# Kernel optimization log

Measured on AMD Instinct MI355X. Metric: run time of the kernel, lower is better.

Reference implementation:

```python
import jax, jax.numpy as jnp
import numpy as np

N = 50000
E = 800000
IN_F = 128
OUT_F = 64
HEADS = 4
NEG_SLOPE = 0.2
EPS = 1e-8


def setup_inputs() -> dict:
    key = jax.random.key(0)
    k1, k2, k3, k4, k5 = jax.random.split(key, 5)
    x = jax.random.normal(k1, (N, IN_F), dtype=jnp.float32)
    edge_index = jax.random.randint(k2, (2, E), 0, N, dtype=jnp.int64)
    # xavier-uniform-like scales
    wb = float(np.sqrt(6.0 / (IN_F + OUT_F)))
    ab = float(np.sqrt(6.0 / (OUT_F + 1)))
    W = jax.random.uniform(k3, (HEADS, IN_F, OUT_F), dtype=jnp.float32, minval=-wb, maxval=wb)
    a_src = jax.random.uniform(k4, (HEADS, OUT_F, 1), dtype=jnp.float32, minval=-ab, maxval=ab)
    a_dst = jax.random.uniform(k5, (HEADS, OUT_F, 1), dtype=jnp.float32, minval=-ab, maxval=ab)
    return {"x": x, "edge_index": edge_index, "W": W, "a_src": a_src, "a_dst": a_dst}


def reference(x, edge_index, W, a_src, a_dst):
    n = x.shape[0]
    src, dst = edge_index[0], edge_index[1]
    # per-head projection: (H, N, F)
    Wh = jnp.einsum('ni,hif->hnf', x, W)
    e_src = jnp.einsum('hnf,hf->hn', Wh, a_src[..., 0])
    e_dst = jnp.einsum('hnf,hf->hn', Wh, a_dst[..., 0])
    e = jax.nn.leaky_relu(e_src[:, src] + e_dst[:, dst], NEG_SLOPE)  # (H, E)
    # edge softmax over destination; original initializes e_max to zeros,
    # so effective max is max(segment_max, 0)
    seg_max = jax.vmap(lambda eh: jax.ops.segment_max(eh, dst, num_segments=n))(e)
    e_max = jnp.maximum(seg_max, 0.0)
    exp_e = jnp.exp(e - e_max[:, dst])
    exp_sum = jax.vmap(lambda ee: jax.ops.segment_sum(ee, dst, num_segments=n))(exp_e)
    att = exp_e / (exp_sum[:, dst] + EPS)  # (H, E); dropout omitted (eval)
    # weighted scatter-add aggregation: (H, E, F) messages -> (H, N, F)
    msgs = att[..., None] * Wh[:, src]
    out = jax.vmap(lambda m: jax.ops.segment_sum(m, dst, num_segments=n))(msgs)
    # concat heads: (N, H*F)
    return out.transpose(1, 0, 2).reshape(n, -1)
```

## Files before the change

kernel.cpp:

```cpp
#include <hip/hip_runtime.h>
#include <hip/hip_bf16.h>

#define N_NODES 50000
#define E_EDGES 800000
#define IN_F    128
#define OUT_F   64
#define HEADS   4
#define HF      (HEADS * OUT_F)
#define NEG_SLOPE 0.2f
#define EPS     1e-8f
#define CAP     64
#define NB_INIT ((N_NODES + 255) / 256)

typedef __attribute__((ext_vector_type(8))) short bf16x8;
typedef __attribute__((ext_vector_type(4))) float f32x4;

__device__ __forceinline__ unsigned short f2bf(float f) {
    return __hip_bfloat16_raw(__float2bfloat16(f)).x;
}
__device__ __forceinline__ float bf2f(unsigned short u) {
    return __uint_as_float((unsigned)u << 16);
}

__global__ __launch_bounds__(256) void wcvt_kernel(
    const float* __restrict__ W,
    short* __restrict__ Wtb,
    int* __restrict__ cnt)
{
    const int i = blockIdx.x * 256 + threadIdx.x;
    if (i < N_NODES) cnt[i] = 0;
    if (i < HEADS * IN_F * OUT_F) {
        const int h  = i >> 13;
        const int fl = (i >> 7) & 63;
        const int k  = i & 127;
        Wtb[i] = (short)f2bf(W[h * (IN_F * OUT_F) + k * OUT_F + fl]);
    }
}

__global__ __launch_bounds__(256) void proj_kernel(
    const float* __restrict__ x,
    const short* __restrict__ Wtb,
    const float* __restrict__ a_src,
    const float* __restrict__ a_dst,
    const int* __restrict__ src,
    const int* __restrict__ dst,
    unsigned short* __restrict__ Whb,
    float* __restrict__ esrc,
    float* __restrict__ edst,
    int* __restrict__ cnt,
    int* __restrict__ csr)
{
    __shared__ short xs[16][136];
    __shared__ unsigned short ot[16][256];

    const int tid = threadIdx.x;
    const int n0 = blockIdx.x * 16;

    const int e  = blockIdx.x * 256 + tid;
    const int de = dst[e];
    const int se = src[e];
    const int pos = atomicAdd(&cnt[de], 1);

    {
        const int row = tid >> 4;
        const int kb = (tid & 15) * 8;
        const float* xp = x + (size_t)(n0 + row) * IN_F + kb;
        const float4 x0 = *(const float4*)(xp);
        const float4 x1 = *(const float4*)(xp + 4);
        bf16x8 v;
        v[0] = (short)f2bf(x0.x); v[1] = (short)f2bf(x0.y);
        v[2] = (short)f2bf(x0.z); v[3] = (short)f2bf(x0.w);
        v[4] = (short)f2bf(x1.x); v[5] = (short)f2bf(x1.y);
        v[6] = (short)f2bf(x1.z); v[7] = (short)f2bf(x1.w);
        *(bf16x8*)&xs[row][kb] = v;
    }
    __syncthreads();

    const int h = tid >> 6;
    const int lane = tid & 63;
    const int c = lane & 15;
    const int quad = lane >> 4;

    bf16x8 a[4];
#pragma unroll
    for (int ks = 0; ks < 4; ++ks)
        a[ks] = *(const bf16x8*)&xs[c][ks * 32 + quad * 8];

    f32x4 acc[4];
#pragma unroll
    for (int nt = 0; nt < 4; ++nt) acc[nt] = (f32x4){0.f, 0.f, 0.f, 0.f};

    const short* Wh_head = Wtb + (h << 13);
#pragma unroll
    for (int nt = 0; nt < 4; ++nt) {
        const short* wrow = Wh_head + ((nt * 16 + c) << 7) + (quad << 3);
#pragma unroll
        for (int ks = 0; ks < 4; ++ks) {
            const bf16x8 b = *(const bf16x8*)(wrow + (ks << 5));
            acc[nt] = __builtin_amdgcn_mfma_f32_16x16x32_bf16(a[ks], b, acc[nt], 0, 0, 0);
        }
    }

    float ps[4] = {0.f, 0.f, 0.f, 0.f};
    float pd[4] = {0.f, 0.f, 0.f, 0.f};
#pragma unroll
    for (int nt = 0; nt < 4; ++nt) {
        const float as = a_src[h * OUT_F + nt * 16 + c];
        const float ad = a_dst[h * OUT_F + nt * 16 + c];
#pragma unroll
        for (int r = 0; r < 4; ++r) {
            ps[r] += acc[nt][r] * as;
            pd[r] += acc[nt][r] * ad;
        }
    }
#pragma unroll
    for (int m = 1; m < 16; m <<= 1) {
#pragma unroll
        for (int r = 0; r < 4; ++r) {
            ps[r] += __shfl_xor(ps[r], m);
            pd[r] += __shfl_xor(pd[r], m);
        }
    }
    if (c == 0) {
#pragma unroll
        for (int r = 0; r < 4; ++r) {
            const int n = n0 + quad * 4 + r;
            esrc[n * HEADS + h] = ps[r];
            edst[n * HEADS + h] = pd[r];
        }
    }

#pragma unroll
    for (int nt = 0; nt < 4; ++nt) {
#pragma unroll
        for (int r = 0; r < 4; ++r)
            ot[quad * 4 + r][(nt * 16 + c) * 4 + h] = f2bf(acc[nt][r]);
    }
    __syncthreads();
    {
        const unsigned short* sp = &ot[0][0] + tid * 16;
        unsigned short* gp = Whb + (size_t)n0 * HF + tid * 16;
        *(int4*)(gp)     = *(const int4*)(sp);
        *(int4*)(gp + 8) = *(const int4*)(sp + 8);
    }

    if (pos < CAP) csr[de * CAP + pos] = se;
}

__global__ __launch_bounds__(256) void aggregate_kernel(
    const int* __restrict__ cnt,
    const int* __restrict__ csr,
    const float* __restrict__ esrc,
    const float* __restrict__ edst,
    const unsigned short* __restrict__ Whb,
    float* __restrict__ out)
{
    __shared__ int   sb[4][64];
    __shared__ float pb[4][64][4];

    const int wid = threadIdx.x >> 6;
    const int lane = threadIdx.x & 63;
    const int d = blockIdx.x * 4 + wid;

    int deg = cnt[d];
    deg = deg > CAP ? CAP : deg;

    const float4 ed4 = *(const float4*)(edst + d * HEADS);
    const unsigned short* wbase = Whb + (lane << 2);

    float l0 = 0.f, l1 = 0.f, l2 = 0.f, l3 = 0.f;
    if (lane < deg) {
        const int s = csr[d * CAP + lane];
        const float4 es4 = *(const float4*)(esrc + s * HEADS);
        float v0 = es4.x + ed4.x; v0 = v0 > 0.f ? v0 : NEG_SLOPE * v0;
        float v1 = es4.y + ed4.y; v1 = v1 > 0.f ? v1 : NEG_SLOPE * v1;
        float v2 = es4.z + ed4.z; v2 = v2 > 0.f ? v2 : NEG_SLOPE * v2;
        float v3 = es4.w + ed4.w; v3 = v3 > 0.f ? v3 : NEG_SLOPE * v3;
        l0 = __expf(v0); l1 = __expf(v1); l2 = __expf(v2); l3 = __expf(v3);
        sb[wid][lane] = s;
        *(float4*)pb[wid][lane] = (float4){l0, l1, l2, l3};
    }

    float o0 = 0.f, o1 = 0.f, o2 = 0.f, o3 = 0.f;
    int i = 0;
    for (; i + 4 <= deg; i += 4) {
        const int s0 = sb[wid][i];
        const int s1 = sb[wid][i + 1];
        const int s2 = sb[wid][i + 2];
        const int s3 = sb[wid][i + 3];
        const float4 q0 = *(const float4*)pb[wid][i];
        const float4 q1 = *(const float4*)pb[wid][i + 1];
        const float4 q2 = *(const float4*)pb[wid][i + 2];
        const float4 q3 = *(const float4*)pb[wid][i + 3];
        const ushort4 w0 = *(const ushort4*)(wbase + (unsigned)s0 * HF);
        const ushort4 w1 = *(const ushort4*)(wbase + (unsigned)s1 * HF);
        const ushort4 w2 = *(const ushort4*)(wbase + (unsigned)s2 * HF);
        const ushort4 w3 = *(const ushort4*)(wbase + (unsigned)s3 * HF);
        o0 += q0.x * bf2f(w0.x) + q1.x * bf2f(w1.x) + q2.x * bf2f(w2.x) + q3.x * bf2f(w3.x);
        o1 += q0.y * bf2f(w0.y) + q1.y * bf2f(w1.y) + q2.y * bf2f(w2.y) + q3.y * bf2f(w3.y);
        o2 += q0.z * bf2f(w0.z) + q1.z * bf2f(w1.z) + q2.z * bf2f(w2.z) + q3.z * bf2f(w3.z);
        o3 += q0.w * bf2f(w0.w) + q1.w * bf2f(w1.w) + q2.w * bf2f(w2.w) + q3.w * bf2f(w3.w);
    }
    for (; i < deg; ++i) {
        const int s0 = sb[wid][i];
        const float4 q0 = *(const float4*)pb[wid][i];
        const ushort4 w0 = *(const ushort4*)(wbase + (unsigned)s0 * HF);
        o0 += q0.x * bf2f(w0.x);
        o1 += q0.y * bf2f(w0.y);
        o2 += q0.z * bf2f(w0.z);
        o3 += q0.w * bf2f(w0.w);
    }

#pragma unroll
    for (int m = 1; m < 64; m <<= 1) {
        l0 += __shfl_xor(l0, m);
        l1 += __shfl_xor(l1, m);
        l2 += __shfl_xor(l2, m);
        l3 += __shfl_xor(l3, m);
    }
    const float r0 = 1.f / (l0 + EPS);
    const float r1 = 1.f / (l1 + EPS);
    const float r2 = 1.f / (l2 + EPS);
    const float r3 = 1.f / (l3 + EPS);

    float* op = out + (size_t)d * HF + lane;
    op[0]   = o0 * r0;
    op[64]  = o1 * r1;
    op[128] = o2 * r2;
    op[192] = o3 * r3;
}

extern "C" void kernel_launch(void* const* d_in, const int* in_sizes, int n_in,
                              void* d_out, int out_size, void* d_ws, size_t ws_size,
                              hipStream_t stream) {
    const float* x      = (const float*)d_in[0];
    const int*   eidx   = (const int*)d_in[1];
    const float* W      = (const float*)d_in[2];
    const float* a_src  = (const float*)d_in[3];
    const float* a_dst  = (const float*)d_in[4];
    float* out = (float*)d_out;

    const int* src = eidx;
    const int* dst = eidx + E_EDGES;

    unsigned short* Whb = (unsigned short*)d_ws;
    float* esrc   = (float*)(Whb + (size_t)N_NODES * HF);
    float* edst   = esrc + (size_t)N_NODES * HEADS;
    int*   cnt    = (int*)(edst + (size_t)N_NODES * HEADS);
    int*   csr    = cnt + N_NODES;
    short* Wtb    = (short*)(csr + (size_t)N_NODES * CAP);

    wcvt_kernel<<<NB_INIT, 256, 0, stream>>>(W, Wtb, cnt);

    proj_kernel<<<N_NODES / 16, 256, 0, stream>>>(x, Wtb, a_src, a_dst, src, dst,
                                                  Whb, esrc, edst, cnt, csr);

    aggregate_kernel<<<N_NODES / 4, 256, 0, stream>>>(cnt, csr, esrc, edst, Whb, out);
}
```

Measured before the change: 197.0 us.

## Switch Wh storage to head-major layout and vectorize aggregate output stores

Result: no change. 193.1 us (-2.0%).

```diff
diff --git a/kernel.cpp b/kernel.cpp
--- a/kernel.cpp
+++ b/kernel.cpp
@@ -51,7 +51,7 @@
     int* __restrict__ csr)
 {
     __shared__ short xs[16][136];
-    __shared__ unsigned short ot[16][256];
+    __shared__ unsigned short ot[4][16][72];
 
     const int tid = threadIdx.x;
     const int n0 = blockIdx.x * 16;
@@ -59,7 +59,6 @@
     const int e  = blockIdx.x * 256 + tid;
     const int de = dst[e];
     const int se = src[e];
-    const int pos = atomicAdd(&cnt[de], 1);
 
     {
         const int row = tid >> 4;
@@ -76,6 +75,8 @@
     }
     __syncthreads();
 
+    const int pos = atomicAdd(&cnt[de], 1);
+
     const int h = tid >> 6;
     const int lane = tid & 63;
     const int c = lane & 15;
@@ -134,17 +135,18 @@
     for (int nt = 0; nt < 4; ++nt) {
 #pragma unroll
         for (int r = 0; r < 4; ++r)
-            ot[quad * 4 + r][(nt * 16 + c) * 4 + h] = f2bf(acc[nt][r]);
-    }
-    __syncthreads();
+            ot[h][quad * 4 + r][nt * 16 + c] = f2bf(acc[nt][r]);
+    }
     {
-        const unsigned short* sp = &ot[0][0] + tid * 16;
-        unsigned short* gp = Whb + (size_t)n0 * HF + tid * 16;
+        const int row = lane >> 2;
+        const int co  = (lane & 3) * 16;
+        unsigned short* gp = Whb + (size_t)(n0 + row) * HF + h * OUT_F + co;
+        const unsigned short* sp = &ot[h][row][co];
         *(int4*)(gp)     = *(const int4*)(sp);
         *(int4*)(gp + 8) = *(const int4*)(sp + 8);
     }
 
-    if (pos < CAP) csr[de * CAP + pos] = se;
+    if (pos < CAP) __builtin_nontemporal_store(se, &csr[de * CAP + pos]);
 }
 
 __global__ __launch_bounds__(256) void aggregate_kernel(
@@ -166,11 +168,12 @@
     deg = deg > CAP ? CAP : deg;
 
     const float4 ed4 = *(const float4*)(edst + d * HEADS);
+    const int h = lane >> 4;
     const unsigned short* wbase = Whb + (lane << 2);
 
     float l0 = 0.f, l1 = 0.f, l2 = 0.f, l3 = 0.f;
     if (lane < deg) {
-        const int s = csr[d * CAP + lane];
+        const int s = __builtin_nontemporal_load(&csr[d * CAP + lane]);
         const float4 es4 = *(const float4*)(esrc + s * HEADS);
         float v0 = es4.x + ed4.x; v0 = v0 > 0.f ? v0 : NEG_SLOPE * v0;
         float v1 = es4.y + ed4.y; v1 = v1 > 0.f ? v1 : NEG_SLOPE * v1;
@@ -183,32 +186,33 @@
 
     float o0 = 0.f, o1 = 0.f, o2 = 0.f, o3 = 0.f;
     int i = 0;
-    for (; i + 4 <= deg; i += 4) {
-        const int s0 = sb[wid][i];
-        const int s1 = sb[wid][i + 1];
-        const int s2 = sb[wid][i + 2];
-        const int s3 = sb[wid][i + 3];
-        const float4 q0 = *(const float4*)pb[wid][i];
-        const float4 q1 = *(const float4*)pb[wid][i + 1];
-        const float4 q2 = *(const float4*)pb[wid][i + 2];
-        const float4 q3 = *(const float4*)pb[wid][i + 3];
-        const ushort4 w0 = *(const ushort4*)(wbase + (unsigned)s0 * HF);
-        const ushort4 w1 = *(const ushort4*)(wbase + (unsigned)s1 * HF);
-        const ushort4 w2 = *(const ushort4*)(wbase + (unsigned)s2 * HF);
-        const ushort4 w3 = *(const ushort4*)(wbase + (unsigned)s3 * HF);
-        o0 += q0.x * bf2f(w0.x) + q1.x * bf2f(w1.x) + q2.x * bf2f(w2.x) + q3.x * bf2f(w3.x);
-        o1 += q0.y * bf2f(w0.y) + q1.y * bf2f(w1.y) + q2.y * bf2f(w2.y) + q3.y * bf2f(w3.y);
-        o2 += q0.z * bf2f(w0.z) + q1.z * bf2f(w1.z) + q2.z * bf2f(w2.z) + q3.z * bf2f(w3.z);
-        o3 += q0.w * bf2f(w0.w) + q1.w * bf2f(w1.w) + q2.w * bf2f(w2.w) + q3.w * bf2f(w3.w);
+    for (; i + 8 <= deg; i += 8) {
+        int s[8];
+#pragma unroll
+        for (int j = 0; j < 8; ++j) s[j] = sb[wid][i + j];
+        ushort4 w[8];
+#pragma unroll
+        for (int j = 0; j < 8; ++j)
+            w[j] = *(const ushort4*)(wbase + (unsigned)s[j] * HF);
+        float q[8];
+#pragma unroll
+        for (int j = 0; j < 8; ++j) q[j] = pb[wid][i + j][h];
+#pragma unroll
+        for (int j = 0; j < 8; ++j) {
+            o0 += q[j] * bf2f(w[j].x);
+            o1 += q[j] * bf2f(w[j].y);
+            o2 += q[j] * bf2f(w[j].z);
+            o3 += q[j] * bf2f(w[j].w);
+        }
     }
     for (; i < deg; ++i) {
         const int s0 = sb[wid][i];
-        const float4 q0 = *(const float4*)pb[wid][i];
+        const float q0 = pb[wid][i][h];
         const ushort4 w0 = *(const ushort4*)(wbase + (unsigned)s0 * HF);
-        o0 += q0.x * bf2f(w0.x);
-        o1 += q0.y * bf2f(w0.y);
-        o2 += q0.z * bf2f(w0.z);
-        o3 += q0.w * bf2f(w0.w);
+        o0 += q0 * bf2f(w0.x);
+        o1 += q0 * bf2f(w0.y);
+        o2 += q0 * bf2f(w0.z);
+        o3 += q0 * bf2f(w0.w);
     }
 
 #pragma unroll
@@ -218,16 +222,11 @@
         l2 += __shfl_xor(l2, m);
         l3 += __shfl_xor(l3, m);
     }
-    const float r0 = 1.f / (l0 + EPS);
-    const float r1 = 1.f / (l1 + EPS);
-    const float r2 = 1.f / (l2 + EPS);
-    const float r3 = 1.f / (l3 + EPS);
-
-    float* op = out + (size_t)d * HF + lane;
-    op[0]   = o0 * r0;
-    op[64]  = o1 * r1;
-    op[128] = o2 * r2;
-    op[192] = o3 * r3;
+    const float lsum = (h == 0) ? l0 : (h == 1) ? l1 : (h == 2) ? l2 : l3;
+    const float r = 1.f / (lsum + EPS);
+
+    const f32x4 o4 = {o0 * r, o1 * r, o2 * r, o3 * r};
+    __builtin_nontemporal_store(o4, (f32x4*)(out + (size_t)d * HF + (lane << 2)));
 }
 
 extern "C" void kernel_launch(void* const* d_in, const int* in_sizes, int n_in,
```
